# Kernel optimization log

Measured on AMD Instinct MI355X. Metric: run time of the kernel, lower is better.

The kernel has to match this reference:

```python
import jax, jax.numpy as jnp
import numpy as np

K = 3            # char conv window (in words of chars)
B, P, LC = 64, 80, 18   # batch, padded sentence len, padded word char len
E = 256          # embedding_dim (shared by word and char embeddings)
H = 1024         # lstm hidden
L_CH = 4         # conv output channels
VOCAB, ALPHA, TAGS = 50000, 100, 50


def setup_inputs() -> dict:
    key = jax.random.key(0)
    ks = jax.random.split(key, 12)
    D = E + L_CH  # lstm input dim
    s = 0.02
    return {
        "sentence_batch": jax.random.randint(ks[0], (B, P), 0, VOCAB),
        "character_batch": jax.random.randint(ks[1], (B, P, LC), 0, ALPHA),
        "word_emb": jax.random.normal(ks[2], (VOCAB, E), jnp.float32) * s,
        "char_emb": jax.random.normal(ks[3], (ALPHA, E), jnp.float32) * s,
        "conv_w": jax.random.normal(ks[4], (L_CH, K * E), jnp.float32) * s,
        "conv_b": jax.random.normal(ks[5], (L_CH,), jnp.float32) * s,
        "w_ih": jax.random.normal(ks[6], (4 * H, D), jnp.float32) * s,
        "w_hh": jax.random.normal(ks[7], (4 * H, H), jnp.float32) * s,
        "b_ih": jax.random.normal(ks[8], (4 * H,), jnp.float32) * s,
        "b_hh": jax.random.normal(ks[9], (4 * H,), jnp.float32) * s,
        "out_w": jax.random.normal(ks[10], (TAGS, H), jnp.float32) * s,
        "out_b": jax.random.normal(ks[11], (TAGS,), jnp.float32) * s,
    }


def reference(sentence_batch, character_batch, word_emb, char_emb, conv_w,
              conv_b, w_ih, w_hh, b_ih, b_hh, out_w, out_b):
    # --- char CNN: sliding K-window over char embeddings, flatten, linear, max ---
    ce = char_emb[character_batch]                      # [B,P,LC,E]
    Wn = LC - K + 1                                     # windows per word
    widx = jnp.arange(Wn)[:, None] + jnp.arange(K)      # [Wn,K]
    win = ce[:, :, widx, :].reshape(B, P, Wn, K * E)    # [B,P,Wn,K*E]
    # Conv1d(in=1, out=4, kernel=K*E) on a length-K*E input == one linear per window
    phi = jnp.einsum('bpwd,cd->bpwc', win, conv_w) + conv_b  # [B,P,Wn,4]
    char_repr = phi.max(axis=2)                         # [B,P,4] (max over windows)

    # --- word embeddings + concat ---
    we = word_emb[sentence_batch]                       # [B,P,E]
    combined = jnp.concatenate([we, char_repr], axis=2) # [B,P,E+4]
    D = combined.shape[-1]
    # faithful to torch: .view(PADDING_SIZE, BATCH_SIZE, -1) is a reshape, not transpose
    x = combined.reshape(P, B, D)                       # [P,B,D]

    # --- LSTM (torch gate order i,f,g,o) ---
    def step(carry, x_t):
        h, c = carry
        gates = x_t @ w_ih.T + b_ih + h @ w_hh.T + b_hh  # [B,4H]
        i, f, g, o = jnp.split(gates, 4, axis=-1)
        i = jax.nn.sigmoid(i)
        f = jax.nn.sigmoid(f)
        g = jnp.tanh(g)
        o = jax.nn.sigmoid(o)
        c = f * c + i * g
        h = o * jnp.tanh(c)
        return (h, c), h

    h0 = jnp.zeros((B, H), x.dtype)
    c0 = jnp.zeros((B, H), x.dtype)
    _, hs = jax.lax.scan(step, (h0, c0), x)             # [P,B,H]

    # faithful reshape back, linear head, log_softmax over dim=1 (the P axis)
    lstm_out = hs.reshape(B, P, H)
    tag_space = lstm_out @ out_w.T + out_b              # [B,P,TAGS]
    return jax.nn.log_softmax(tag_space, axis=1)
```

## Files before the change

### kernel.cpp

```cpp
#include <hip/hip_runtime.h>
#include <math.h>

#define BB 64
#define PP 80
#define LC 18
#define EE 256
#define HH 1024
#define LCH 4
#define KW 3
#define TAGS 50
#define DD 260
#define KPAD 288
#define ROWS (BB*PP)
#define WN (LC-KW+1)
#define NG (4*HH)
#define GRP 4
#define NBLK (GRP*64)
#define HSTEP32 (GRP*32*512)

typedef __attribute__((ext_vector_type(8))) short short8;
typedef __attribute__((ext_vector_type(4))) short short4v;
typedef __attribute__((ext_vector_type(4))) float floatx4;
typedef __attribute__((ext_vector_type(4))) int int4v;

__device__ __forceinline__ short f2bf(float x) {
    unsigned u = __float_as_uint(x);
    unsigned r = (u + 0x7FFFu + ((u >> 16) & 1u)) >> 16;
    return (short)r;
}
__device__ __forceinline__ float bf2f(short s) {
    return __uint_as_float(((unsigned)(unsigned short)s) << 16);
}
__device__ __forceinline__ float sigf(float x) { return 1.f / (1.f + __expf(-x)); }
__device__ __forceinline__ float tanhfast(float x) {
    float e = __expf(2.f * x);
    return 1.f - 2.f / (e + 1.f);
}
__device__ __forceinline__ float wave_reduce_sum(float v) {
    for (int off = 32; off > 0; off >>= 1) v += __shfl_xor(v, off, 64);
    return v;
}

__global__ __launch_bounds__(256) void prep_kernel(
    const float* __restrict__ wih, const float* __restrict__ whh,
    const float* __restrict__ outw,
    short* __restrict__ wih_bf, short* __restrict__ wpk,
    short* __restrict__ outw_bf, unsigned* __restrict__ hst32)
{
    const int NI = NG * KPAD;
    const int NH = NG * HH;
    const int NO = 64 * HH;
    const int total = NI + NH + NO;
    for (int i = blockIdx.x * 256 + threadIdx.x; i < total; i += gridDim.x * 256) {
        if (i < NI) {
            int r = i / KPAD, c = i - r * KPAD;
            wih_bf[i] = (c < DD) ? f2bf(wih[r * DD + c]) : (short)0;
        } else if (i < NI + NH) {
            int o = i - NI;
            int e  = o & 7;
            int l  = (o >> 3) & 63;
            int s  = (o >> 9) & 3;
            int tl = (o >> 11) & 3;
            int w  = (o >> 13) & 7;
            int bl = o >> 16;
            int row = tl * HH + bl * 16 + (l & 15);
            int col = w * 128 + s * 32 + (l >> 4) * 8 + e;
            wpk[o] = f2bf(whh[(size_t)row * HH + col]);
        } else {
            int k = i - NI - NH;
            int r = k >> 10;
            outw_bf[k] = (r < TAGS) ? f2bf(outw[k]) : (short)0;
        }
    }
    int4v z = {0, 0, 0, 0};
    int4v* hz = (int4v*)hst32;
    const int NZ = PP * HSTEP32 / 4;
    for (int i = blockIdx.x * 256 + threadIdx.x; i < NZ; i += gridDim.x * 256)
        hz[i] = z;
}

__global__ __launch_bounds__(256) void embed_kernel(
    const int* __restrict__ sent, const int* __restrict__ chars,
    const float* __restrict__ word_emb, const float* __restrict__ char_emb,
    const float* __restrict__ conv_w, const float* __restrict__ conv_b,
    short* __restrict__ X)
{
    __shared__ float4 ce[LC * 64];
    __shared__ float phi[WN * LCH];
    __shared__ float charrep[LCH];
    const int r = blockIdx.x;
    const int t = threadIdx.x;
    const int lane = t & 63, wv = t >> 6;

    const int cbase = r * LC;
    for (int i = 0; i < 5; ++i) {
        int idx = i * 256 + t;
        if (idx < LC * 64) {
            int j = idx >> 6, e4 = idx & 63;
            int ch = chars[cbase + j];
            ce[idx] = ((const float4*)(char_emb + (size_t)ch * EE))[e4];
        }
    }
    float4 cw[KW][LCH];
    #pragma unroll
    for (int k = 0; k < KW; ++k)
        #pragma unroll
        for (int c = 0; c < LCH; ++c)
            cw[k][c] = ((const float4*)(conv_w + c * (KW * EE) + k * EE))[lane];
    __syncthreads();

    #pragma unroll
    for (int wi = 0; wi < 4; ++wi) {
        int w = wv + wi * 4;
        float acc[LCH] = {0.f, 0.f, 0.f, 0.f};
        #pragma unroll
        for (int k = 0; k < KW; ++k) {
            float4 v = ce[(w + k) * 64 + lane];
            #pragma unroll
            for (int c = 0; c < LCH; ++c)
                acc[c] += v.x * cw[k][c].x + v.y * cw[k][c].y +
                          v.z * cw[k][c].z + v.w * cw[k][c].w;
        }
        #pragma unroll
        for (int c = 0; c < LCH; ++c) {
            float s = wave_reduce_sum(acc[c]);
            if (lane == 0) phi[w * LCH + c] = s;
        }
    }
    __syncthreads();
    if (t < LCH) {
        float m = -1e30f;
        for (int w = 0; w < WN; ++w) m = fmaxf(m, phi[w * LCH + t]);
        charrep[t] = m + conv_b[t];
    }
    __syncthreads();

    const int word = sent[r];
    X[(size_t)r * KPAD + t] = f2bf(word_emb[(size_t)word * EE + t]);
    if (t < LCH) X[(size_t)r * KPAD + EE + t] = f2bf(charrep[t]);
    if (t >= 228) X[(size_t)r * KPAD + 32 + t] = (short)0;
}

__global__ __launch_bounds__(256) void gemm_in_kernel(
    const short* __restrict__ X, const short* __restrict__ Wih,
    const float* __restrict__ b_ih, const float* __restrict__ b_hh,
    short* __restrict__ ginP)
{
    const int tid = threadIdx.x;
    const int l = tid & 63, wv = tid >> 6;
    const int r0 = blockIdx.x * 64;
    const int n0 = blockIdx.y * 128 + wv * 32;
    const int lr = l & 15, lh = l >> 4;

    floatx4 acc[4][2];
    #pragma unroll
    for (int m = 0; m < 4; ++m)
        #pragma unroll
        for (int n = 0; n < 2; ++n) acc[m][n] = (floatx4)0.f;

    const short* Xb = X + (size_t)(r0 + lr) * KPAD + lh * 8;
    const short* Wb = Wih + (size_t)(n0 + lr) * KPAD + lh * 8;

    #pragma unroll
    for (int k0 = 0; k0 < KPAD; k0 += 32) {
        short8 a0 = *(const short8*)(Xb + k0);
        short8 a1 = *(const short8*)(Xb + 16 * KPAD + k0);
        short8 a2 = *(const short8*)(Xb + 32 * KPAD + k0);
        short8 a3 = *(const short8*)(Xb + 48 * KPAD + k0);
        short8 b0 = *(const short8*)(Wb + k0);
        short8 b1 = *(const short8*)(Wb + 16 * KPAD + k0);
        acc[0][0] = __builtin_amdgcn_mfma_f32_16x16x32_bf16(a0, b0, acc[0][0], 0, 0, 0);
        acc[1][0] = __builtin_amdgcn_mfma_f32_16x16x32_bf16(a1, b0, acc[1][0], 0, 0, 0);
        acc[2][0] = __builtin_amdgcn_mfma_f32_16x16x32_bf16(a2, b0, acc[2][0], 0, 0, 0);
        acc[3][0] = __builtin_amdgcn_mfma_f32_16x16x32_bf16(a3, b0, acc[3][0], 0, 0, 0);
        acc[0][1] = __builtin_amdgcn_mfma_f32_16x16x32_bf16(a0, b1, acc[0][1], 0, 0, 0);
        acc[1][1] = __builtin_amdgcn_mfma_f32_16x16x32_bf16(a1, b1, acc[1][1], 0, 0, 0);
        acc[2][1] = __builtin_amdgcn_mfma_f32_16x16x32_bf16(a2, b1, acc[2][1], 0, 0, 0);
        acc[3][1] = __builtin_amdgcn_mfma_f32_16x16x32_bf16(a3, b1, acc[3][1], 0, 0, 0);
    }
    #pragma unroll
    for (int m = 0; m < 4; ++m)
        #pragma unroll
        for (int n = 0; n < 2; ++n) {
            int col = n0 + n * 16 + lr;
            float bias = b_ih[col] + b_hh[col];
            short4v pack;
            #pragma unroll
            for (int q = 0; q < 4; ++q) pack[q] = f2bf(acc[m][n][q] + bias);
            int w_ = col >> 10, bl_ = (col >> 4) & 63, uu_ = col & 15;
            size_t addr = ((((size_t)(blockIdx.x * GRP + m) * 64 + bl_) * 4 + w_) * 16
                           + uu_) * 16 + lh * 4;
            *(short4v*)(ginP + addr) = pack;
        }
}

__global__ __launch_bounds__(512, 1) void lstm_seq_kernel(
    unsigned* __restrict__ hst, const short* __restrict__ wpk,
    const short* __restrict__ ginP)
{
    __shared__ __align__(16) float lds_g[8][4][16][20];
    __shared__ __align__(16) unsigned hbuf32[16][20];

    const int tid = threadIdx.x;
    const int l = tid & 63;
    const int w = tid >> 6;
    const int g  = blockIdx.x >> 6;
    const int bl = blockIdx.x & 63;

    short8 barr[4][4];
    {
        const short* wb = wpk + ((size_t)(bl * 8 + w) * 16) * 512 + l * 8;
        #pragma unroll
        for (int tl = 0; tl < 4; ++tl)
            #pragma unroll
            for (int s = 0; s < 4; ++s)
                barr[tl][s] = *(const short8*)(wb + (tl * 4 + s) * 512);
    }

    const int b16 = tid & 15;
    const int uu  = (tid >> 4) & 15;
    float c = 0.f;

    const int seg = w * 8 + (l & 7);
    const int s_lr = seg & 15, s_hl = (seg >> 4) & 1, s_eh = seg >> 5;
    const int s_ll = (2 * (bl & 1) + s_hl) * 16 + s_lr;
    const size_t s_off = (size_t)g * 16384 + (size_t)(bl >> 1) * 512 + s_ll * 8 + s_eh * 4;

    float gv[4] = {0.f, 0.f, 0.f, 0.f};
    if (tid < 256) {
        const short* gb = ginP + (((size_t)g * 64 + bl) * 4) * 256 + uu * 16 + b16;
        #pragma unroll
        for (int q = 0; q < 4; ++q) gv[q] = bf2f(gb[q * 256]);
    }

    for (int t = 0; t < PP; ++t) {
        if (t > 0) {
            const unsigned* A = hst + (size_t)(t - 1) * HSTEP32 + g * 16384
                                + (w * 4) * 512 + l * 8;
            int4v d[8];
            int ok;
            do {
                #pragma unroll
                for (int s = 0; s < 4; ++s) {
                    asm volatile("global_load_dwordx4 %0, %1, off sc0 sc1"
                                 : "=v"(d[2 * s]) : "v"(A + s * 512) : "memory");
                    asm volatile("global_load_dwordx4 %0, %1, off sc0 sc1"
                                 : "=v"(d[2 * s + 1]) : "v"(A + s * 512 + 4) : "memory");
                }
                asm volatile("s_waitcnt vmcnt(0)" ::: "memory");
                __builtin_amdgcn_sched_barrier(0);
                ok = 1;
                #pragma unroll
                for (int i = 0; i < 8; ++i)
                    #pragma unroll
                    for (int j = 0; j < 4; ++j)
                        ok &= ((((unsigned)d[i][j]) & 0xFFFFu) == (unsigned)t);
                ok = __all(ok);
                if (!ok) __builtin_amdgcn_s_sleep(2);
            } while (!ok);

            floatx4 acc[4];
            #pragma unroll
            for (int tl = 0; tl < 4; ++tl) acc[tl] = (floatx4)0.f;
            #pragma unroll
            for (int s = 0; s < 4; ++s) {
                int4v pk;
                pk[0] = (int)((((unsigned)d[2*s][0]) >> 16)   | (((unsigned)d[2*s][1])   & 0xFFFF0000u));
                pk[1] = (int)((((unsigned)d[2*s][2]) >> 16)   | (((unsigned)d[2*s][3])   & 0xFFFF0000u));
                pk[2] = (int)((((unsigned)d[2*s+1][0]) >> 16) | (((unsigned)d[2*s+1][1]) & 0xFFFF0000u));
                pk[3] = (int)((((unsigned)d[2*s+1][2]) >> 16) | (((unsigned)d[2*s+1][3]) & 0xFFFF0000u));
                short8 av = __builtin_bit_cast(short8, pk);
                #pragma unroll
                for (int tl = 0; tl < 4; ++tl)
                    acc[tl] = __builtin_amdgcn_mfma_f32_16x16x32_bf16(
                        av, barr[tl][s], acc[tl], 0, 0, 0);
            }
            #pragma unroll
            for (int tl = 0; tl < 4; ++tl)
                *(floatx4*)&lds_g[w][tl][l & 15][(l >> 4) * 4] = acc[tl];
            __syncthreads();
        }

        if (tid < 256) {
            float s0 = gv[0], s1 = gv[1], s2 = gv[2], s3 = gv[3];
            if (t > 0) {
                #pragma unroll
                for (int w2 = 0; w2 < 8; ++w2) {
                    s0 += lds_g[w2][0][uu][b16];
                    s1 += lds_g[w2][1][uu][b16];
                    s2 += lds_g[w2][2][uu][b16];
                    s3 += lds_g[w2][3][uu][b16];
                }
            }
            float i_ = sigf(s0), f_ = sigf(s1), g_ = tanhfast(s2), o_ = sigf(s3);
            c = f_ * c + i_ * g_;
            unsigned hd = (((unsigned)(unsigned short)f2bf(o_ * tanhfast(c))) << 16)
                          | (unsigned)(t + 1);
            hbuf32[b16][uu] = hd;

            if (t + 1 < PP) {
                const short* gb = ginP + (((size_t)(t + 1) * GRP + g) * 64 + bl) * 1024
                                  + uu * 16 + b16;
                #pragma unroll
                for (int q = 0; q < 4; ++q) gv[q] = bf2f(gb[q * 256]);
            }
        }
        __syncthreads();

        if ((l & 56) == 0) {
            int4v hv = *(const int4v*)&hbuf32[s_lr][s_hl * 8 + s_eh * 4];
            unsigned* hp = hst + (size_t)t * HSTEP32 + s_off;
            asm volatile("global_store_dwordx4 %0, %1, off sc0 sc1"
                         :: "v"(hp), "v"(hv) : "memory");
        }
    }
}

__global__ __launch_bounds__(256) void tag_kernel(
    const unsigned* __restrict__ hst, const short* __restrict__ outw_bf,
    const float* __restrict__ out_b, float* __restrict__ out)
{
    const int tid = threadIdx.x;
    const int l = tid & 63, wv = tid >> 6;
    const int t = blockIdx.x;
    const int n0 = wv * 16;
    const int lr = l & 15, lh = l >> 4;

    const unsigned* At = hst + (size_t)t * HSTEP32;
    const short* Bw = outw_bf + (size_t)(n0 + lr) * HH + lh * 8;

    floatx4 acc[4];
    #pragma unroll
    for (int m = 0; m < 4; ++m) acc[m] = (floatx4)0.f;

    #pragma unroll 4
    for (int kk = 0; kk < 32; ++kk) {
        short8 b = *(const short8*)(Bw + kk * 32);
        #pragma unroll
        for (int m = 0; m < 4; ++m) {
            const unsigned* ap = At + m * 16384 + kk * 512 + l * 8;
            int4v d0 = *(const int4v*)(ap);
            int4v d1 = *(const int4v*)(ap + 4);
            int4v pk;
            pk[0] = (int)((((unsigned)d0[0]) >> 16) | (((unsigned)d0[1]) & 0xFFFF0000u));
            pk[1] = (int)((((unsigned)d0[2]) >> 16) | (((unsigned)d0[3]) & 0xFFFF0000u));
            pk[2] = (int)((((unsigned)d1[0]) >> 16) | (((unsigned)d1[1]) & 0xFFFF0000u));
            pk[3] = (int)((((unsigned)d1[2]) >> 16) | (((unsigned)d1[3]) & 0xFFFF0000u));
            short8 a = __builtin_bit_cast(short8, pk);
            acc[m] = __builtin_amdgcn_mfma_f32_16x16x32_bf16(a, b, acc[m], 0, 0, 0);
        }
    }
    int col = n0 + lr;
    if (col < TAGS) {
        float bias = out_b[col];
        #pragma unroll
        for (int m = 0; m < 4; ++m)
            #pragma unroll
            for (int q = 0; q < 4; ++q) {
                int row = t * 64 + m * 16 + lh * 4 + q;
                out[(size_t)row * TAGS + col] = acc[m][q] + bias;
            }
    }
}

__global__ __launch_bounds__(256) void logsoftmax_kernel(float* __restrict__ out)
{
    const int tid = threadIdx.x;
    const int lane = tid & 63;
    const int pair = blockIdx.x * 4 + (tid >> 6);
    if (pair >= BB * TAGS) return;
    const int bb = pair / TAGS, g = pair % TAGS;
    float* base = out + (size_t)bb * PP * TAGS + g;
    float v0 = base[lane * TAGS];
    float v1 = (lane < PP - 64) ? base[(lane + 64) * TAGS] : -1e30f;
    float m = fmaxf(v0, v1);
    for (int off = 32; off > 0; off >>= 1) m = fmaxf(m, __shfl_xor(m, off, 64));
    float s = __expf(v0 - m) + ((lane < PP - 64) ? __expf(v1 - m) : 0.f);
    s = wave_reduce_sum(s);
    float lz = m + __logf(s);
    base[lane * TAGS] = v0 - lz;
    if (lane < PP - 64) base[(lane + 64) * TAGS] = v1 - lz;
}

extern "C" void kernel_launch(void* const* d_in, const int* in_sizes, int n_in,
                              void* d_out, int out_size, void* d_ws, size_t ws_size,
                              hipStream_t stream)
{
    const int*   sent     = (const int*)d_in[0];
    const int*   chars    = (const int*)d_in[1];
    const float* word_emb = (const float*)d_in[2];
    const float* char_emb = (const float*)d_in[3];
    const float* conv_w   = (const float*)d_in[4];
    const float* conv_b   = (const float*)d_in[5];
    const float* w_ih     = (const float*)d_in[6];
    const float* w_hh     = (const float*)d_in[7];
    const float* b_ih     = (const float*)d_in[8];
    const float* b_hh     = (const float*)d_in[9];
    const float* out_w    = (const float*)d_in[10];
    const float* out_b    = (const float*)d_in[11];
    float* out = (float*)d_out;

    short* X_bf     = (short*)d_ws;
    short* wih_bf   = X_bf + (size_t)ROWS * KPAD;
    short* wpk      = wih_bf + (size_t)NG * KPAD;
    short* outw_bf  = wpk + (size_t)NG * HH;
    short* ginP     = outw_bf + (size_t)64 * HH;
    unsigned* hst32 = (unsigned*)(ginP + (size_t)NG * ROWS);

    hipLaunchKernelGGL(prep_kernel, dim3(2048), dim3(256), 0, stream,
                       w_ih, w_hh, out_w, wih_bf, wpk, outw_bf, hst32);
    hipLaunchKernelGGL(embed_kernel, dim3(ROWS), dim3(256), 0, stream,
                       sent, chars, word_emb, char_emb, conv_w, conv_b, X_bf);
    hipLaunchKernelGGL(gemm_in_kernel, dim3(ROWS / 64, NG / 128), dim3(256), 0, stream,
                       X_bf, wih_bf, b_ih, b_hh, ginP);
    {
        void* kargs[3] = { (void*)&hst32, (void*)&wpk, (void*)&ginP };
        hipLaunchCooperativeKernel((void*)lstm_seq_kernel, dim3(NBLK), dim3(512),
                                   kargs, 0, stream);
    }
    hipLaunchKernelGGL(tag_kernel, dim3(PP), dim3(256), 0, stream,
                       hst32, outw_bf, out_b, out);
    hipLaunchKernelGGL(logsoftmax_kernel, dim3((BB * TAGS + 3) / 4), dim3(256), 0, stream,
                       out);
}
```

Before: 458.4 us.

## Halve LSTM recurrence block count with 32 hidden units per block

Each persistent LSTM block now owns 32 hidden units instead of 16, so there are half as many blocks (128 vs 256) and each wave holds twice the recurrent weight tiles in registers. All 512 threads now take part in the gate nonlinearities, and the h-publish store is simplified to contiguous 512-element chunks per block. The spin-wait now re-polls only the h segments that are still stale, and its sleep is shorter. The change aims to cut cross-block synchronisation traffic and polling cost, at the price of doubling register pressure for the B fragments and doubling the MFMA work per block per step.

```diff
diff --git a/kernel.cpp b/kernel.cpp
--- a/kernel.cpp
+++ b/kernel.cpp
@@ -15,7 +15,8 @@
 #define WN (LC-KW+1)
 #define NG (4*HH)
 #define GRP 4
-#define NBLK (GRP*64)
+#define UPB 32
+#define NBLK (GRP*(HH/UPB))
 #define HSTEP32 (GRP*32*512)
 
 typedef __attribute__((ext_vector_type(8))) short short8;
@@ -60,10 +61,10 @@
             int e  = o & 7;
             int l  = (o >> 3) & 63;
             int s  = (o >> 9) & 3;
-            int tl = (o >> 11) & 3;
-            int w  = (o >> 13) & 7;
-            int bl = o >> 16;
-            int row = tl * HH + bl * 16 + (l & 15);
+            int tl = (o >> 11) & 7;
+            int w  = (o >> 14) & 7;
+            int bl = o >> 17;
+            int row = (tl >> 1) * HH + bl * 32 + (tl & 1) * 16 + (l & 15);
             int col = w * 128 + s * 32 + (l >> 4) * 8 + e;
             wpk[o] = f2bf(whh[(size_t)row * HH + col]);
         } else {
@@ -198,37 +199,34 @@
     unsigned* __restrict__ hst, const short* __restrict__ wpk,
     const short* __restrict__ ginP)
 {
-    __shared__ __align__(16) float lds_g[8][4][16][20];
-    __shared__ __align__(16) unsigned hbuf32[16][20];
+    __shared__ __align__(16) float lds_g[8][8][16][20];
+    __shared__ __align__(16) unsigned hbuf32[64][12];
 
     const int tid = threadIdx.x;
     const int l = tid & 63;
     const int w = tid >> 6;
-    const int g  = blockIdx.x >> 6;
-    const int bl = blockIdx.x & 63;
-
-    short8 barr[4][4];
+    const int g  = blockIdx.x >> 5;
+    const int bl = blockIdx.x & 31;
+
+    short8 barr[8][4];
     {
-        const short* wb = wpk + ((size_t)(bl * 8 + w) * 16) * 512 + l * 8;
-        #pragma unroll
-        for (int tl = 0; tl < 4; ++tl)
+        const short* wb = wpk + (size_t)(bl * 8 + w) * 16384 + l * 8;
+        #pragma unroll
+        for (int tl = 0; tl < 8; ++tl)
             #pragma unroll
             for (int s = 0; s < 4; ++s)
-                barr[tl][s] = *(const short8*)(wb + (tl * 4 + s) * 512);
+                barr[tl][s] = *(const short8*)(wb + tl * 2048 + s * 512);
     }
 
     const int b16 = tid & 15;
-    const int uu  = (tid >> 4) & 15;
+    const int uu  = tid >> 4;
+    const int U_  = bl * 32 + uu;
     float c = 0.f;
 
-    const int seg = w * 8 + (l & 7);
-    const int s_lr = seg & 15, s_hl = (seg >> 4) & 1, s_eh = seg >> 5;
-    const int s_ll = (2 * (bl & 1) + s_hl) * 16 + s_lr;
-    const size_t s_off = (size_t)g * 16384 + (size_t)(bl >> 1) * 512 + s_ll * 8 + s_eh * 4;
-
-    float gv[4] = {0.f, 0.f, 0.f, 0.f};
-    if (tid < 256) {
-        const short* gb = ginP + (((size_t)g * 64 + bl) * 4) * 256 + uu * 16 + b16;
+    float gv[4];
+    {
+        const short* gb = ginP + (((size_t)g * 64 + (U_ >> 4)) * 4) * 256
+                          + (U_ & 15) * 16 + b16;
         #pragma unroll
         for (int q = 0; q < 4; ++q) gv[q] = bf2f(gb[q * 256]);
     }
@@ -238,30 +236,36 @@
             const unsigned* A = hst + (size_t)(t - 1) * HSTEP32 + g * 16384
                                 + (w * 4) * 512 + l * 8;
             int4v d[8];
-            int ok;
+            unsigned stale = 0xFu;
             do {
                 #pragma unroll
-                for (int s = 0; s < 4; ++s) {
-                    asm volatile("global_load_dwordx4 %0, %1, off sc0 sc1"
-                                 : "=v"(d[2 * s]) : "v"(A + s * 512) : "memory");
-                    asm volatile("global_load_dwordx4 %0, %1, off sc0 sc1"
-                                 : "=v"(d[2 * s + 1]) : "v"(A + s * 512 + 4) : "memory");
-                }
+                for (int s = 0; s < 4; ++s)
+                    if (stale & (1u << s)) {
+                        asm volatile("global_load_dwordx4 %0, %1, off sc0 sc1"
+                                     : "=v"(d[2 * s]) : "v"(A + s * 512) : "memory");
+                        asm volatile("global_load_dwordx4 %0, %1, off sc0 sc1"
+                                     : "=v"(d[2 * s + 1]) : "v"(A + s * 512 + 4) : "memory");
+                    }
                 asm volatile("s_waitcnt vmcnt(0)" ::: "memory");
                 __builtin_amdgcn_sched_barrier(0);
-                ok = 1;
                 #pragma unroll
-                for (int i = 0; i < 8; ++i)
-                    #pragma unroll
-                    for (int j = 0; j < 4; ++j)
-                        ok &= ((((unsigned)d[i][j]) & 0xFFFFu) == (unsigned)t);
-                ok = __all(ok);
-                if (!ok) __builtin_amdgcn_s_sleep(2);
-            } while (!ok);
-
-            floatx4 acc[4];
-            #pragma unroll
-            for (int tl = 0; tl < 4; ++tl) acc[tl] = (floatx4)0.f;
+                for (int s = 0; s < 4; ++s)
+                    if (stale & (1u << s)) {
+                        int ok = 1;
+                        #pragma unroll
+                        for (int i = 0; i < 2; ++i)
+                            #pragma unroll
+                            for (int j = 0; j < 4; ++j)
+                                ok &= ((((unsigned)d[2 * s + i][j]) & 0xFFFFu)
+                                       == (unsigned)t);
+                        if (__all(ok)) stale &= ~(1u << s);
+                    }
+                if (stale) __builtin_amdgcn_s_sleep(1);
+            } while (stale);
+
+            floatx4 acc[8];
+            #pragma unroll
+            for (int tl = 0; tl < 8; ++tl) acc[tl] = (floatx4)0.f;
             #pragma unroll
             for (int s = 0; s < 4; ++s) {
                 int4v pk;
@@ -271,45 +275,47 @@
                 pk[3] = (int)((((unsigned)d[2*s+1][2]) >> 16) | (((unsigned)d[2*s+1][3]) & 0xFFFF0000u));
                 short8 av = __builtin_bit_cast(short8, pk);
                 #pragma unroll
-                for (int tl = 0; tl < 4; ++tl)
+                for (int tl = 0; tl < 8; ++tl)
                     acc[tl] = __builtin_amdgcn_mfma_f32_16x16x32_bf16(
                         av, barr[tl][s], acc[tl], 0, 0, 0);
             }
             #pragma unroll
-            for (int tl = 0; tl < 4; ++tl)
+            for (int tl = 0; tl < 8; ++tl)
                 *(floatx4*)&lds_g[w][tl][l & 15][(l >> 4) * 4] = acc[tl];
             __syncthreads();
         }
 
-        if (tid < 256) {
+        {
             float s0 = gv[0], s1 = gv[1], s2 = gv[2], s3 = gv[3];
             if (t > 0) {
                 #pragma unroll
                 for (int w2 = 0; w2 < 8; ++w2) {
-                    s0 += lds_g[w2][0][uu][b16];
-                    s1 += lds_g[w2][1][uu][b16];
-                    s2 += lds_g[w2][2][uu][b16];
-                    s3 += lds_g[w2][3][uu][b16];
+                    s0 += lds_g[w2][0 + (uu >> 4)][uu & 15][b16];
+                    s1 += lds_g[w2][2 + (uu >> 4)][uu & 15][b16];
+                    s2 += lds_g[w2][4 + (uu >> 4)][uu & 15][b16];
+                    s3 += lds_g[w2][6 + (uu >> 4)][uu & 15][b16];
                 }
             }
             float i_ = sigf(s0), f_ = sigf(s1), g_ = tanhfast(s2), o_ = sigf(s3);
             c = f_ * c + i_ * g_;
             unsigned hd = (((unsigned)(unsigned short)f2bf(o_ * tanhfast(c))) << 16)
                           | (unsigned)(t + 1);
-            hbuf32[b16][uu] = hd;
+            hbuf32[(uu >> 3) * 16 + b16][uu & 7] = hd;
 
             if (t + 1 < PP) {
-                const short* gb = ginP + (((size_t)(t + 1) * GRP + g) * 64 + bl) * 1024
-                                  + uu * 16 + b16;
+                const short* gb = ginP + ((((size_t)(t + 1) * GRP + g) * 64
+                                          + (U_ >> 4)) * 4) * 256 + (U_ & 15) * 16 + b16;
                 #pragma unroll
                 for (int q = 0; q < 4; ++q) gv[q] = bf2f(gb[q * 256]);
             }
         }
         __syncthreads();
 
-        if ((l & 56) == 0) {
-            int4v hv = *(const int4v*)&hbuf32[s_lr][s_hl * 8 + s_eh * 4];
-            unsigned* hp = hst + (size_t)t * HSTEP32 + s_off;
+        if (tid < 128) {
+            int lane_ = tid >> 1, e0 = (tid & 1) * 4;
+            int4v hv = *(const int4v*)&hbuf32[lane_][e0];
+            unsigned* hp = hst + (size_t)t * HSTEP32 + g * 16384 + bl * 512
+                           + lane_ * 8 + e0;
             asm volatile("global_store_dwordx4 %0, %1, off sc0 sc1"
                          :: "v"(hp), "v"(hv) : "memory");
         }
```

Measured after the change: 463.8 us. About the same (+1.2%).
